# Optimization experiments

Measured on AMD Instinct MI355X. Metric: run time of the kernel, lower is better.

## Reference

```python
import jax, jax.numpy as jnp
import numpy as np
from jax import lax

K = 2048  # nb_subsampled_points


def setup_inputs() -> dict:
    key = jax.random.key(0)
    k1, k2 = jax.random.split(key)
    B, N, D = 32, 131072, 3
    x = jax.random.normal(k1, (B, N, D), dtype=jnp.float32)
    start_idx = jax.random.randint(k2, (B,), 0, N, dtype=jnp.int64)
    return {"x": x, "start_idx": start_idx}


def reference(x, start_idx):
    """Iterative farthest point sampling.

    x: [B, N, D] point cloud, start_idx: [B] initial centroid indices.
    Returns [B, K] int indices of the sampled centroids.
    """
    B, N, D = x.shape

    def step(carry, _):
        min_d, idx = carry                                   # [B,N], [B]
        centroid = jnp.take_along_axis(x, idx[:, None, None], axis=1)  # [B,1,D]
        dist = jnp.sqrt(jnp.sum((x - centroid) ** 2, axis=2))          # [B,N]
        min_d = jnp.minimum(min_d, dist)
        next_idx = jnp.argmax(min_d, axis=1)                 # farthest point
        return (min_d, next_idx), idx

    init = (jnp.full((B, N), jnp.inf, dtype=x.dtype), start_idx.astype(jnp.int32))
    _, idxs = lax.scan(step, init, None, length=K)           # [K, B]
    return idxs.T                                            # [B, K]
```

## Files before the change

### kernel.cpp

```cpp
#include <hip/hip_runtime.h>

#define NB 32
#define NPTS 131072
#define KSAMP 2048
#define NPART 8
#define TPB 512
#define NPT 32
#define PART_PTS (NPTS / NPART)
#define BATCH_F (NPTS * 3)
#define SOA_BYTES ((size_t)NB * BATCH_F * 4)


#define GRP8(X) X(0)X(1)X(2)X(3)X(4)X(5)X(6)X(7)
#define RPT32(X) X(0)X(1)X(2)X(3)X(4)X(5)X(6)X(7)X(8)X(9)X(10)X(11)X(12) \
  X(13)X(14)X(15)X(16)X(17)X(18)X(19)X(20)X(21)X(22)X(23)X(24)X(25)X(26) \
  X(27)X(28)X(29)X(30)X(31)

__device__ __forceinline__ int read_start(const int* start, int b) {
  bool is64 = true;
  #pragma unroll 1
  for (int i = 1; i < 32; i += 2) {
    if (start[i] != 0) { is64 = false; break; }
  }
  return is64 ? start[2 * b] : start[b];
}

__global__ __launch_bounds__(256) void repack_kernel(
    const float* __restrict__ x, float* __restrict__ W)
{
  const int blk = blockIdx.x;
  const int b   = blk >> 6;
  const int c   = blk & 63;
  const int t   = threadIdx.x;
  const float* xb = x + (size_t)b * BATCH_F;
  float* X = W + (size_t)b * BATCH_F;
  float* Y = X + NPTS;
  float* Z = Y + NPTS;
  #pragma unroll
  for (int i = 0; i < 8; ++i) {
    const int n = c * 2048 + i * 256 + t;
    X[n] = xb[3 * n + 0];
    Y[n] = xb[3 * n + 1];
    Z[n] = xb[3 * n + 2];
  }
}

__global__ __launch_bounds__(TPB, 2) void fps_soa(
    const float* __restrict__ W, const int* __restrict__ start,
    int* __restrict__ out, unsigned long long* __restrict__ slot)
{
  #pragma clang fp contract(off)
  const int blk  = blockIdx.x;
  const int xcd  = blk & 7;
  const int j    = blk >> 3;
  const int b    = xcd * 4 + (j & 3);
  const int part = j >> 2;
  const int tid  = threadIdx.x;
  const int lane = tid & 63;
  const int wave = tid >> 6;

  const float* Xb = W + (size_t)b * BATCH_F;
  const float* Yb = Xb + NPTS;
  const float* Zb = Yb + NPTS;

  int cur = read_start(start, b);
  const int S = part * PART_PTS;

  const float4* Xt = (const float4*)(Xb + S) + wave * 512 + lane;
  const float4* Yt = (const float4*)(Yb + S) + wave * 512 + lane;
  const float4* Zt = (const float4*)(Zb + S) + wave * 512 + lane;
  const int nbase = S + wave * 2048 + lane * 4;

  #define DECLG(G) float md2_##G##_0 = __builtin_inff(),  \
      md2_##G##_1 = __builtin_inff(),                     \
      md2_##G##_2 = __builtin_inff(),                     \
      md2_##G##_3 = __builtin_inff();
  GRP8(DECLG)

  __shared__ unsigned long long wred[TPB / 64];
  __shared__ int snext;

  if (part == 0 && tid == 0) out[b * KSAMP] = cur;

  float cx = Xb[cur], cy = Yb[cur], cz = Zb[cur];

  unsigned long long* const srow0 = slot + (size_t)b * 2 * NPART;

  for (int k = 0; k < KSAMP - 1; ++k) {
    float bestv = -1.0f;
    int   bestn = 0;
    #define SC(G,I,XX,YY,ZZ) {                                  \
      const float dx = (XX) - cx;                               \
      const float dy = (YY) - cy;                               \
      const float dz = (ZZ) - cz;                               \
      const float d2 = fmaf(dz, dz, fmaf(dx, dx, dy * dy));     \
      const float m  = fminf(md2_##G##_##I, d2);                \
      md2_##G##_##I = m;                                        \
      if (m > bestv) { bestv = m; bestn = nbase + (G)*256 + (I); } }
    #define SCANG(G) {                                          \
      const float4 xv = Xt[(G) * 64];                           \
      const float4 yv = Yt[(G) * 64];                           \
      const float4 zv = Zt[(G) * 64];                           \
      SC(G,0,xv.x,yv.x,zv.x)                                    \
      SC(G,1,xv.y,yv.y,zv.y)                                    \
      SC(G,2,xv.z,yv.z,zv.z)                                    \
      SC(G,3,xv.w,yv.w,zv.w) }
    GRP8(SCANG)

    const float sdw = sqrtf(bestv);

    unsigned long long key =
        ((unsigned long long)__float_as_uint(sdw) << 32) |
        (unsigned int)(NPTS - 1 - bestn);

    #pragma unroll
    for (int off = 32; off >= 1; off >>= 1) {
      unsigned long long o = __shfl_xor(key, off, 64);
      if (o > key) key = o;
    }
    if (lane == 0) wred[wave] = key;
    __syncthreads();

    if (wave == 0) {
      unsigned long long v = wred[lane & 7];
      #pragma unroll
      for (int off = 4; off >= 1; off >>= 1) {
        unsigned long long o = __shfl_xor(v, off, 64);
        if (o > v) v = o;
      }

      const unsigned tag = (unsigned)(k + 1);
      unsigned long long* const row = srow0 + (unsigned)(k & 1) * NPART;
      if (lane == 0)
        __hip_atomic_store(&row[part], v | ((unsigned long long)tag << 17),
                           __ATOMIC_RELAXED, __HIP_MEMORY_SCOPE_AGENT);

      unsigned long long g;
      do {
        g = __hip_atomic_load(&row[lane & (NPART - 1)], __ATOMIC_RELAXED,
                              __HIP_MEMORY_SCOPE_AGENT);
      } while (__ballot(((unsigned)(g >> 17) & 0x7FFFu) == tag) != ~0ull);

      #pragma unroll
      for (int off = 4; off >= 1; off >>= 1) {
        unsigned long long o = __shfl_xor(g, off, 64);
        if (o > g) g = o;
      }
      const int nidx = NPTS - 1 - (int)(g & 0x1FFFFu);
      if (lane == 0) {
        snext = nidx;
        if (part == 0) out[b * KSAMP + k + 1] = nidx;
      }
    }
    __syncthreads();

    const int nidx = snext;
    cx = Xb[nidx];
    cy = Yb[nidx];
    cz = Zb[nidx];
  }
}

__global__ __launch_bounds__(TPB)
__attribute__((amdgpu_waves_per_eu(2, 2)))
void fps_aos(
    const float* __restrict__ x, const int* __restrict__ start,
    int* __restrict__ out, unsigned long long* __restrict__ slot)
{
  #pragma clang fp contract(off)
  const int blk  = blockIdx.x;
  const int xcd  = blk & 7;
  const int j    = blk >> 3;
  const int b    = xcd * 4 + (j & 3);
  const int part = j >> 2;
  const int tid  = threadIdx.x;
  const int lane = tid & 63;
  const int wave = tid >> 6;

  const float* xb = x + (size_t)b * BATCH_F;
  int cur = read_start(start, b);
  const int base = part * PART_PTS + tid;

  #define DECLP(J) float px##J, py##J, pz##J, md2##J;
  RPT32(DECLP)
  #define INITP(J) { const int n = base + (J) * TPB;          \
      px##J = xb[3*n]; py##J = xb[3*n+1]; pz##J = xb[3*n+2];  \
      md2##J = __builtin_inff(); }
  RPT32(INITP)

  __shared__ unsigned long long wred[TPB / 64];
  __shared__ int snext;

  if (part == 0 && tid == 0) out[b * KSAMP] = cur;

  float cx = xb[3 * (size_t)cur + 0];
  float cy = xb[3 * (size_t)cur + 1];
  float cz = xb[3 * (size_t)cur + 2];

  unsigned long long* const srow0 = slot + (size_t)b * 2 * NPART;

  for (int k = 0; k < KSAMP - 1; ++k) {
    float bestv = -1.0f;
    int   bestn = 0;
    #define SCANP(J) {                                              \
      const float dx = px##J - cx;                                  \
      const float dy = py##J - cy;                                  \
      const float dz = pz##J - cz;                                  \
      const float d2 = fmaf(dz, dz, fmaf(dx, dx, dy * dy));         \
      const float m  = fminf(md2##J, d2);                           \
      md2##J = m;                                                   \
      if (m > bestv) { bestv = m; bestn = base + (J) * TPB; }       \
    }
    RPT32(SCANP)

    const float sdw = sqrtf(bestv);

    unsigned long long key =
        ((unsigned long long)__float_as_uint(sdw) << 32) |
        (unsigned int)(NPTS - 1 - bestn);

    #pragma unroll
    for (int off = 32; off >= 1; off >>= 1) {
      unsigned long long o = __shfl_xor(key, off, 64);
      if (o > key) key = o;
    }
    if (lane == 0) wred[wave] = key;
    __syncthreads();

    if (wave == 0) {
      unsigned long long v = wred[lane & 7];
      #pragma unroll
      for (int off = 4; off >= 1; off >>= 1) {
        unsigned long long o = __shfl_xor(v, off, 64);
        if (o > v) v = o;
      }
      const unsigned tag = (unsigned)(k + 1);
      unsigned long long* const row = srow0 + (unsigned)(k & 1) * NPART;
      if (lane == 0)
        __hip_atomic_store(&row[part], v | ((unsigned long long)tag << 17),
                           __ATOMIC_RELAXED, __HIP_MEMORY_SCOPE_AGENT);

      unsigned long long g;
      do {
        g = __hip_atomic_load(&row[lane & (NPART - 1)], __ATOMIC_RELAXED,
                              __HIP_MEMORY_SCOPE_AGENT);
      } while (__ballot(((unsigned)(g >> 17) & 0x7FFFu) == tag) != ~0ull);

      #pragma unroll
      for (int off = 4; off >= 1; off >>= 1) {
        unsigned long long o = __shfl_xor(g, off, 64);
        if (o > g) g = o;
      }
      const int nidx = NPTS - 1 - (int)(g & 0x1FFFFu);
      if (lane == 0) {
        snext = nidx;
        if (part == 0) out[b * KSAMP + k + 1] = nidx;
      }
    }
    __syncthreads();

    const int nidx = snext;
    cx = xb[3 * (size_t)nidx + 0];
    cy = xb[3 * (size_t)nidx + 1];
    cz = xb[3 * (size_t)nidx + 2];
  }
}

extern "C" void kernel_launch(void* const* d_in, const int* in_sizes, int n_in,
                              void* d_out, int out_size, void* d_ws, size_t ws_size,
                              hipStream_t stream) {
  const float* x     = (const float*)d_in[0];
  const int*   start = (const int*)d_in[1];
  int*         out   = (int*)d_out;

  if (ws_size >= SOA_BYTES + 4096) {
    float* W = (float*)d_ws;
    unsigned long long* slot = (unsigned long long*)((char*)d_ws + SOA_BYTES);
    repack_kernel<<<dim3(NB * 64), dim3(256), 0, stream>>>(x, W);
    void* args[] = {(void*)&W, (void*)&start, (void*)&out, (void*)&slot};
    hipLaunchCooperativeKernel((void*)fps_soa, dim3(NB * NPART), dim3(TPB),
                               args, 0, stream);
  } else {
    unsigned long long* slot = (unsigned long long*)d_ws;
    void* args[] = {(void*)&x, (void*)&start, (void*)&out, (void*)&slot};
    hipLaunchCooperativeKernel((void*)fps_aos, dim3(NB * NPART), dim3(TPB),
                               args, 0, stream);
  }
}
```

Measured before the change: 4.879 ms.

## Keep X/Y in LDS, stream Z from global, broadcast centroid coords via slots

Each block now holds its partition's X and Y coordinates in shared memory (128 KB), so only Z is repacked and read from global memory on every iteration. The cross-block exchange also carries the winning centroid's coordinates, packed into three tagged 64-bit slots per partition, so the dependent global load of the next centroid is gone. The aim is to cut per-iteration global/L2 traffic and the latency on the serial critical path. In exchange each block needs a large LDS allocation, which limits occupancy to one block per CU, and each block publishes and polls three slots per iteration instead of one.

After: 6.700 ms. 37.3% more time.

```diff
diff --git a/kernel.cpp b/kernel.cpp
--- a/kernel.cpp
+++ b/kernel.cpp
@@ -5,10 +5,10 @@
 #define KSAMP 2048
 #define NPART 8
 #define TPB 512
-#define NPT 32
 #define PART_PTS (NPTS / NPART)
 #define BATCH_F (NPTS * 3)
-#define SOA_BYTES ((size_t)NB * BATCH_F * 4)
+#define ZW_BYTES ((size_t)NB * NPTS * 4)
+#define SLOT_OFF (ZW_BYTES)
 
 
 #define GRP8(X) X(0)X(1)X(2)X(3)X(4)X(5)X(6)X(7)
@@ -25,29 +25,26 @@
   return is64 ? start[2 * b] : start[b];
 }
 
-__global__ __launch_bounds__(256) void repack_kernel(
-    const float* __restrict__ x, float* __restrict__ W)
+__global__ __launch_bounds__(256) void repack_z(
+    const float* __restrict__ x, float* __restrict__ Zw)
 {
   const int blk = blockIdx.x;
   const int b   = blk >> 6;
   const int c   = blk & 63;
   const int t   = threadIdx.x;
   const float* xb = x + (size_t)b * BATCH_F;
-  float* X = W + (size_t)b * BATCH_F;
-  float* Y = X + NPTS;
-  float* Z = Y + NPTS;
+  float* Zb = Zw + (size_t)b * NPTS;
   #pragma unroll
   for (int i = 0; i < 8; ++i) {
     const int n = c * 2048 + i * 256 + t;
-    X[n] = xb[3 * n + 0];
-    Y[n] = xb[3 * n + 1];
-    Z[n] = xb[3 * n + 2];
-  }
-}
-
-__global__ __launch_bounds__(TPB, 2) void fps_soa(
-    const float* __restrict__ W, const int* __restrict__ start,
-    int* __restrict__ out, unsigned long long* __restrict__ slot)
+    Zb[n] = xb[3 * n + 2];
+  }
+}
+
+__global__ __launch_bounds__(TPB) void fps_lds(
+    const float* __restrict__ x, const float* __restrict__ Zw,
+    const int* __restrict__ start, int* __restrict__ out,
+    unsigned long long* __restrict__ slot)
 {
   #pragma clang fp contract(off)
   const int blk  = blockIdx.x;
@@ -59,17 +56,28 @@
   const int lane = tid & 63;
   const int wave = tid >> 6;
 
-  const float* Xb = W + (size_t)b * BATCH_F;
-  const float* Yb = Xb + NPTS;
-  const float* Zb = Yb + NPTS;
+  const float* xb = x + (size_t)b * BATCH_F;
+  const float* Zb = Zw + (size_t)b * NPTS;
+  const int S = part * PART_PTS;
+
+  __shared__ float Xl[PART_PTS];
+  __shared__ float Yl[PART_PTS];
+  __shared__ unsigned long long wkey[TPB / 64];
+  __shared__ float wx[TPB / 64], wy[TPB / 64], wz[TPB / 64];
+  __shared__ float bc[3];
 
   int cur = read_start(start, b);
-  const int S = part * PART_PTS;
-
-  const float4* Xt = (const float4*)(Xb + S) + wave * 512 + lane;
-  const float4* Yt = (const float4*)(Yb + S) + wave * 512 + lane;
-  const float4* Zt = (const float4*)(Zb + S) + wave * 512 + lane;
-  const int nbase = S + wave * 2048 + lane * 4;
+
+  #pragma unroll
+  for (int g = 0; g < 8; ++g) {
+    #pragma unroll
+    for (int i = 0; i < 4; ++i) {
+      const int q = g * 2048 + tid * 4 + i;
+      const int n = S + q;
+      Xl[q] = xb[3 * n + 0];
+      Yl[q] = xb[3 * n + 1];
+    }
+  }
 
   #define DECLG(G) float md2_##G##_0 = __builtin_inff(),  \
       md2_##G##_1 = __builtin_inff(),                     \
@@ -77,14 +85,15 @@
       md2_##G##_3 = __builtin_inff();
   GRP8(DECLG)
 
-  __shared__ unsigned long long wred[TPB / 64];
-  __shared__ int snext;
-
   if (part == 0 && tid == 0) out[b * KSAMP] = cur;
 
-  float cx = Xb[cur], cy = Yb[cur], cz = Zb[cur];
-
-  unsigned long long* const srow0 = slot + (size_t)b * 2 * NPART;
+  float cx = xb[3 * (size_t)cur + 0];
+  float cy = xb[3 * (size_t)cur + 1];
+  float cz = xb[3 * (size_t)cur + 2];
+
+  unsigned long long* const srow0 = slot + (size_t)b * 2 * NPART * 3;
+
+  __syncthreads();
 
   for (int k = 0; k < KSAMP - 1; ++k) {
     float bestv = -1.0f;
@@ -96,68 +105,106 @@
       const float d2 = fmaf(dz, dz, fmaf(dx, dx, dy * dy));     \
       const float m  = fminf(md2_##G##_##I, d2);                \
       md2_##G##_##I = m;                                        \
-      if (m > bestv) { bestv = m; bestn = nbase + (G)*256 + (I); } }
-    #define SCANG(G) {                                          \
-      const float4 xv = Xt[(G) * 64];                           \
-      const float4 yv = Yt[(G) * 64];                           \
-      const float4 zv = Zt[(G) * 64];                           \
-      SC(G,0,xv.x,yv.x,zv.x)                                    \
-      SC(G,1,xv.y,yv.y,zv.y)                                    \
-      SC(G,2,xv.z,yv.z,zv.z)                                    \
+      if (m > bestv) { bestv = m; bestn = S + (G)*2048 + tid*4 + (I); } }
+    #define SCANG(G) {                                                      \
+      const float4 xv = *reinterpret_cast<const float4*>(&Xl[(G)*2048 + tid*4]); \
+      const float4 yv = *reinterpret_cast<const float4*>(&Yl[(G)*2048 + tid*4]); \
+      const float4 zv = *reinterpret_cast<const float4*>(Zb + S + (G)*2048 + tid*4); \
+      SC(G,0,xv.x,yv.x,zv.x)                                                \
+      SC(G,1,xv.y,yv.y,zv.y)                                                \
+      SC(G,2,xv.z,yv.z,zv.z)                                                \
       SC(G,3,xv.w,yv.w,zv.w) }
     GRP8(SCANG)
 
+    const int bq = bestn - S;
+    float cnx = Xl[bq];
+    float cny = Yl[bq];
+    float cnz = Zb[bestn];
+
     const float sdw = sqrtf(bestv);
-
     unsigned long long key =
         ((unsigned long long)__float_as_uint(sdw) << 32) |
         (unsigned int)(NPTS - 1 - bestn);
 
     #pragma unroll
     for (int off = 32; off >= 1; off >>= 1) {
-      unsigned long long o = __shfl_xor(key, off, 64);
-      if (o > key) key = o;
-    }
-    if (lane == 0) wred[wave] = key;
+      unsigned long long ok = __shfl_xor(key, off, 64);
+      float ox = __shfl_xor(cnx, off, 64);
+      float oy = __shfl_xor(cny, off, 64);
+      float oz = __shfl_xor(cnz, off, 64);
+      if (ok > key) { key = ok; cnx = ox; cny = oy; cnz = oz; }
+    }
+    if (lane == 0) {
+      wkey[wave] = key; wx[wave] = cnx; wy[wave] = cny; wz[wave] = cnz;
+    }
     __syncthreads();
 
+    const unsigned tag = (unsigned)(k + 1);
+    unsigned long long* const row = srow0 + (unsigned)(k & 1) * (NPART * 3);
+
     if (wave == 0) {
-      unsigned long long v = wred[lane & 7];
+      unsigned long long v = wkey[lane & 7];
+      float fx = wx[lane & 7], fy = wy[lane & 7], fz = wz[lane & 7];
       #pragma unroll
       for (int off = 4; off >= 1; off >>= 1) {
-        unsigned long long o = __shfl_xor(v, off, 64);
-        if (o > v) v = o;
-      }
-
-      const unsigned tag = (unsigned)(k + 1);
-      unsigned long long* const row = srow0 + (unsigned)(k & 1) * NPART;
-      if (lane == 0)
-        __hip_atomic_store(&row[part], v | ((unsigned long long)tag << 17),
-                           __ATOMIC_RELAXED, __HIP_MEMORY_SCOPE_AGENT);
-
+        unsigned long long ok = __shfl_xor(v, off, 64);
+        float ox = __shfl_xor(fx, off, 64);
+        float oy = __shfl_xor(fy, off, 64);
+        float oz = __shfl_xor(fz, off, 64);
+        if (ok > v) { v = ok; fx = ox; fy = oy; fz = oz; }
+      }
+
+      if (lane == 0) {
+        const unsigned zb = __float_as_uint(fz);
+        const unsigned long long tg = (unsigned long long)tag << 17;
+        unsigned long long A = v | tg;
+        unsigned long long B = ((unsigned long long)__float_as_uint(fx) << 32)
+                               | tg | (zb & 0x1FFFFu);
+        unsigned long long C = ((unsigned long long)__float_as_uint(fy) << 32)
+                               | tg | (zb >> 17);
+        __hip_atomic_store(&row[part * 3 + 0], A, __ATOMIC_RELAXED,
+                           __HIP_MEMORY_SCOPE_AGENT);
+        __hip_atomic_store(&row[part * 3 + 1], B, __ATOMIC_RELAXED,
+                           __HIP_MEMORY_SCOPE_AGENT);
+        __hip_atomic_store(&row[part * 3 + 2], C, __ATOMIC_RELAXED,
+                           __HIP_MEMORY_SCOPE_AGENT);
+      }
+
+      const int pidx = (lane < 24) ? ((lane & 7) * 3 + (lane >> 3)) : 0;
       unsigned long long g;
       do {
-        g = __hip_atomic_load(&row[lane & (NPART - 1)], __ATOMIC_RELAXED,
+        g = __hip_atomic_load(&row[pidx], __ATOMIC_RELAXED,
                               __HIP_MEMORY_SCOPE_AGENT);
-      } while (__ballot(((unsigned)(g >> 17) & 0x7FFFu) == tag) != ~0ull);
-
+      } while (__ballot(lane >= 24 ||
+                        (((unsigned)(g >> 17) & 0x7FFFu) == tag)) != ~0ull);
+
+      unsigned long long kk = (lane < 8) ? g : 0ull;
       #pragma unroll
       for (int off = 4; off >= 1; off >>= 1) {
-        unsigned long long o = __shfl_xor(g, off, 64);
-        if (o > g) g = o;
-      }
-      const int nidx = NPTS - 1 - (int)(g & 0x1FFFFu);
+        unsigned long long o = __shfl_xor(kk, off, 64);
+        if (o > kk) kk = o;
+      }
+      const unsigned long long bk = __shfl(kk, 0, 64);
+      const unsigned long long mask = __ballot(lane < 8 && g == bk);
+      const int w = __ffsll((unsigned long long)mask) - 1;
+
+      const unsigned long long Bw = __shfl(g, 8 + w, 64);
+      const unsigned long long Cw = __shfl(g, 16 + w, 64);
+      const unsigned zbits = (unsigned)(Bw & 0x1FFFFu) |
+                             ((unsigned)(Cw & 0x7FFFu) << 17);
       if (lane == 0) {
-        snext = nidx;
-        if (part == 0) out[b * KSAMP + k + 1] = nidx;
+        bc[0] = __uint_as_float((unsigned)(Bw >> 32));
+        bc[1] = __uint_as_float((unsigned)(Cw >> 32));
+        bc[2] = __uint_as_float(zbits);
+        if (part == 0)
+          out[b * KSAMP + k + 1] = NPTS - 1 - (int)(bk & 0x1FFFFu);
       }
     }
     __syncthreads();
 
-    const int nidx = snext;
-    cx = Xb[nidx];
-    cy = Yb[nidx];
-    cz = Zb[nidx];
+    cx = bc[0];
+    cy = bc[1];
+    cz = bc[2];
   }
 }
 
@@ -214,7 +261,6 @@
     RPT32(SCANP)
 
     const float sdw = sqrtf(bestv);
-
     unsigned long long key =
         ((unsigned long long)__float_as_uint(sdw) << 32) |
         (unsigned int)(NPTS - 1 - bestn);
@@ -273,12 +319,13 @@
   const int*   start = (const int*)d_in[1];
   int*         out   = (int*)d_out;
 
-  if (ws_size >= SOA_BYTES + 4096) {
-    float* W = (float*)d_ws;
-    unsigned long long* slot = (unsigned long long*)((char*)d_ws + SOA_BYTES);
-    repack_kernel<<<dim3(NB * 64), dim3(256), 0, stream>>>(x, W);
-    void* args[] = {(void*)&W, (void*)&start, (void*)&out, (void*)&slot};
-    hipLaunchCooperativeKernel((void*)fps_soa, dim3(NB * NPART), dim3(TPB),
+  if (ws_size >= ZW_BYTES + 16384) {
+    float* Zw = (float*)d_ws;
+    unsigned long long* slot = (unsigned long long*)((char*)d_ws + SLOT_OFF);
+    repack_z<<<dim3(NB * 64), dim3(256), 0, stream>>>(x, Zw);
+    void* args[] = {(void*)&x, (void*)&Zw, (void*)&start, (void*)&out,
+                    (void*)&slot};
+    hipLaunchCooperativeKernel((void*)fps_lds, dim3(NB * NPART), dim3(TPB),
                                args, 0, stream);
   } else {
     unsigned long long* slot = (unsigned long long*)d_ws;
```

## Keep X/Y coordinates in LDS, stream only Z from global workspace

Applied to the files above, without the earlier changes.

The FPS kernel now loads each block's partition of X and Y coordinates into shared memory once (128 KB of LDS per block) and repacks only Z into a global SoA buffer. Each iteration reads X/Y from LDS and Z from global/L2, which cuts per-iteration global traffic by two thirds. The trade-off is that the large LDS footprint limits occupancy to one block per CU and drops the two-blocks-per-CU launch bound. Centroid coordinates are now fetched from the original AoS input.

Result: no change. 4.936 ms (+1.2%).

```diff
diff --git a/kernel.cpp b/kernel.cpp
--- a/kernel.cpp
+++ b/kernel.cpp
@@ -5,10 +5,10 @@
 #define KSAMP 2048
 #define NPART 8
 #define TPB 512
-#define NPT 32
 #define PART_PTS (NPTS / NPART)
 #define BATCH_F (NPTS * 3)
-#define SOA_BYTES ((size_t)NB * BATCH_F * 4)
+#define ZW_BYTES ((size_t)NB * NPTS * 4)
+#define SLOT_OFF (ZW_BYTES)
 
 
 #define GRP8(X) X(0)X(1)X(2)X(3)X(4)X(5)X(6)X(7)
@@ -25,29 +25,26 @@
   return is64 ? start[2 * b] : start[b];
 }
 
-__global__ __launch_bounds__(256) void repack_kernel(
-    const float* __restrict__ x, float* __restrict__ W)
+__global__ __launch_bounds__(256) void repack_z(
+    const float* __restrict__ x, float* __restrict__ Zw)
 {
   const int blk = blockIdx.x;
   const int b   = blk >> 6;
   const int c   = blk & 63;
   const int t   = threadIdx.x;
   const float* xb = x + (size_t)b * BATCH_F;
-  float* X = W + (size_t)b * BATCH_F;
-  float* Y = X + NPTS;
-  float* Z = Y + NPTS;
+  float* Zb = Zw + (size_t)b * NPTS;
   #pragma unroll
   for (int i = 0; i < 8; ++i) {
     const int n = c * 2048 + i * 256 + t;
-    X[n] = xb[3 * n + 0];
-    Y[n] = xb[3 * n + 1];
-    Z[n] = xb[3 * n + 2];
-  }
-}
-
-__global__ __launch_bounds__(TPB, 2) void fps_soa(
-    const float* __restrict__ W, const int* __restrict__ start,
-    int* __restrict__ out, unsigned long long* __restrict__ slot)
+    Zb[n] = xb[3 * n + 2];
+  }
+}
+
+__global__ __launch_bounds__(TPB) void fps_lds(
+    const float* __restrict__ x, const float* __restrict__ Zw,
+    const int* __restrict__ start, int* __restrict__ out,
+    unsigned long long* __restrict__ slot)
 {
   #pragma clang fp contract(off)
   const int blk  = blockIdx.x;
@@ -59,17 +56,27 @@
   const int lane = tid & 63;
   const int wave = tid >> 6;
 
-  const float* Xb = W + (size_t)b * BATCH_F;
-  const float* Yb = Xb + NPTS;
-  const float* Zb = Yb + NPTS;
+  const float* xb = x + (size_t)b * BATCH_F;
+  const float* Zb = Zw + (size_t)b * NPTS;
+  const int S = part * PART_PTS;
+
+  __shared__ float Xl[PART_PTS];
+  __shared__ float Yl[PART_PTS];
+  __shared__ unsigned long long wred[TPB / 64];
+  __shared__ int snext;
 
   int cur = read_start(start, b);
-  const int S = part * PART_PTS;
-
-  const float4* Xt = (const float4*)(Xb + S) + wave * 512 + lane;
-  const float4* Yt = (const float4*)(Yb + S) + wave * 512 + lane;
-  const float4* Zt = (const float4*)(Zb + S) + wave * 512 + lane;
-  const int nbase = S + wave * 2048 + lane * 4;
+
+  #pragma unroll
+  for (int g = 0; g < 8; ++g) {
+    #pragma unroll
+    for (int i = 0; i < 4; ++i) {
+      const int q = g * 2048 + tid * 4 + i;
+      const int n = S + q;
+      Xl[q] = xb[3 * n + 0];
+      Yl[q] = xb[3 * n + 1];
+    }
+  }
 
   #define DECLG(G) float md2_##G##_0 = __builtin_inff(),  \
       md2_##G##_1 = __builtin_inff(),                     \
@@ -77,14 +84,15 @@
       md2_##G##_3 = __builtin_inff();
   GRP8(DECLG)
 
-  __shared__ unsigned long long wred[TPB / 64];
-  __shared__ int snext;
-
   if (part == 0 && tid == 0) out[b * KSAMP] = cur;
 
-  float cx = Xb[cur], cy = Yb[cur], cz = Zb[cur];
+  float cx = xb[3 * (size_t)cur + 0];
+  float cy = xb[3 * (size_t)cur + 1];
+  float cz = xb[3 * (size_t)cur + 2];
 
   unsigned long long* const srow0 = slot + (size_t)b * 2 * NPART;
+
+  __syncthreads();
 
   for (int k = 0; k < KSAMP - 1; ++k) {
     float bestv = -1.0f;
@@ -96,19 +104,18 @@
       const float d2 = fmaf(dz, dz, fmaf(dx, dx, dy * dy));     \
       const float m  = fminf(md2_##G##_##I, d2);                \
       md2_##G##_##I = m;                                        \
-      if (m > bestv) { bestv = m; bestn = nbase + (G)*256 + (I); } }
-    #define SCANG(G) {                                          \
-      const float4 xv = Xt[(G) * 64];                           \
-      const float4 yv = Yt[(G) * 64];                           \
-      const float4 zv = Zt[(G) * 64];                           \
-      SC(G,0,xv.x,yv.x,zv.x)                                    \
-      SC(G,1,xv.y,yv.y,zv.y)                                    \
-      SC(G,2,xv.z,yv.z,zv.z)                                    \
+      if (m > bestv) { bestv = m; bestn = S + (G)*2048 + tid*4 + (I); } }
+    #define SCANG(G) {                                                      \
+      const float4 xv = *reinterpret_cast<const float4*>(&Xl[(G)*2048 + tid*4]); \
+      const float4 yv = *reinterpret_cast<const float4*>(&Yl[(G)*2048 + tid*4]); \
+      const float4 zv = *reinterpret_cast<const float4*>(Zb + S + (G)*2048 + tid*4); \
+      SC(G,0,xv.x,yv.x,zv.x)                                                \
+      SC(G,1,xv.y,yv.y,zv.y)                                                \
+      SC(G,2,xv.z,yv.z,zv.z)                                                \
       SC(G,3,xv.w,yv.w,zv.w) }
     GRP8(SCANG)
 
     const float sdw = sqrtf(bestv);
-
     unsigned long long key =
         ((unsigned long long)__float_as_uint(sdw) << 32) |
         (unsigned int)(NPTS - 1 - bestn);
@@ -155,9 +162,9 @@
     __syncthreads();
 
     const int nidx = snext;
-    cx = Xb[nidx];
-    cy = Yb[nidx];
-    cz = Zb[nidx];
+    cx = xb[3 * (size_t)nidx + 0];
+    cy = xb[3 * (size_t)nidx + 1];
+    cz = xb[3 * (size_t)nidx + 2];
   }
 }
 
@@ -214,7 +221,6 @@
     RPT32(SCANP)
 
     const float sdw = sqrtf(bestv);
-
     unsigned long long key =
         ((unsigned long long)__float_as_uint(sdw) << 32) |
         (unsigned int)(NPTS - 1 - bestn);
@@ -273,12 +279,13 @@
   const int*   start = (const int*)d_in[1];
   int*         out   = (int*)d_out;
 
-  if (ws_size >= SOA_BYTES + 4096) {
-    float* W = (float*)d_ws;
-    unsigned long long* slot = (unsigned long long*)((char*)d_ws + SOA_BYTES);
-    repack_kernel<<<dim3(NB * 64), dim3(256), 0, stream>>>(x, W);
-    void* args[] = {(void*)&W, (void*)&start, (void*)&out, (void*)&slot};
-    hipLaunchCooperativeKernel((void*)fps_soa, dim3(NB * NPART), dim3(TPB),
+  if (ws_size >= ZW_BYTES + 16384) {
+    float* Zw = (float*)d_ws;
+    unsigned long long* slot = (unsigned long long*)((char*)d_ws + SLOT_OFF);
+    repack_z<<<dim3(NB * 64), dim3(256), 0, stream>>>(x, Zw);
+    void* args[] = {(void*)&x, (void*)&Zw, (void*)&start, (void*)&out,
+                    (void*)&slot};
+    hipLaunchCooperativeKernel((void*)fps_lds, dim3(NB * NPART), dim3(TPB),
                                args, 0, stream);
   } else {
     unsigned long long* slot = (unsigned long long*)d_ws;
```
